# Performance work log

Measured on AMD Instinct MI355X. Metric: run time of the kernel, lower is better.

The kernel has to match this reference:

```python
import jax, jax.numpy as jnp
import numpy as np

N, MUL, NUM_ELEM = 2048, 128, 10
D_IN = 9                      # single-copy input irreps 0e+1o+2e -> 1+3+5
IN_DIMS = (1, 3, 5)           # per-irrep dims of irreps_in
OUT_DIMS = (1, 3)             # per-irrep dims of irreps_out (0e, 1o)
OUT_SLICES = ((0, 1), (1, 4)) # slices into per-mul output of width 4
# (nu, out_idx, n_basis) entries, mirroring reduced_symmetric_tensor_product_basis
ENTRIES = ((1, 0, 1), (1, 1, 1), (2, 0, 3), (2, 1, 2), (3, 0, 4), (3, 1, 2))


def setup_inputs() -> dict:
    key = jax.random.key(0)
    ks = jax.random.split(key, 2 + 2 * len(ENTRIES))
    inp = {}
    inp["node_feats"] = jax.random.normal(ks[0], (N, MUL * D_IN), dtype=jnp.float32)
    inp["species"] = jax.random.randint(ks[1], (N,), 0, NUM_ELEM)
    for i, (nu, oi, nb) in enumerate(ENTRIES):
        d = OUT_DIMS[oi]
        inp[f"basis{i}"] = jax.random.normal(ks[2 + 2 * i], (D_IN,) * nu + (nb, d), dtype=jnp.float32)
        inp[f"weight{i}"] = jax.random.normal(ks[3 + 2 * i], (NUM_ELEM, nb, MUL), dtype=jnp.float32) * (1.0 / np.sqrt(nb))
    return inp


def _to_per_mul(x):
    # (N, sum mul*dim) -> (N, mul, 9)
    pieces, off = [], 0
    for d in IN_DIMS:
        pieces.append(x[:, off:off + MUL * d].reshape(-1, MUL, d))
        off += MUL * d
    return jnp.concatenate(pieces, axis=-1)


def _from_per_mul(x):
    # (N, mul, 4) -> (N, mul*1 + mul*3)
    pieces = []
    for oi, d in enumerate(OUT_DIMS):
        lo, hi = OUT_SLICES[oi]
        pieces.append(x[:, :, lo:hi].reshape(-1, MUL * d))
    return jnp.concatenate(pieces, axis=-1)


def _forward(node_feats, bases, weights, species):
    feats = _to_per_mul(node_feats)                         # (N, mul, 9)
    out = jnp.zeros((feats.shape[0], MUL, 4), dtype=feats.dtype)
    for i, (nu, oi, nb) in enumerate(ENTRIES):
        basis = jax.lax.stop_gradient(bases[i]).astype(feats.dtype)
        tmp = jnp.einsum('a...,nma->nm...', basis, feats)   # (N, mul, 9^(nu-1), nb, d)
        for _ in range(nu - 1):
            tmp = jnp.einsum('nma...,nma->nm...', tmp, feats)
        w = weights[i][species]                             # (N, nb, mul) per-species gather
        contracted = jnp.einsum('nsm,nmsp->nmp', w, tmp)    # (N, mul, d)
        lo, hi = OUT_SLICES[oi]
        out = out.at[:, :, lo:hi].add(contracted)
    return _from_per_mul(out)


def reference(node_feats, species, basis0, weight0, basis1, weight1, basis2, weight2,
              basis3, weight3, basis4, weight4, basis5, weight5):
    bases = [basis0, basis1, basis2, basis3, basis4, basis5]
    weights = [weight0, weight1, weight2, weight3, weight4, weight5]
    return _forward(node_feats, bases, weights, species)
```

## Files before the change

### kernel.cpp

```cpp
#include <hip/hip_runtime.h>


#define N_NODES 2048
#define MUL     128
#define NROW    1152
#define NQ      45
#define NC      165
#define KSPLIT  57
#define Q4_BASE 12
#define C4_BASE 147
#define S4_TOTAL 642

__global__ void k_prep(const float* __restrict__ b0, const float* __restrict__ b1,
                       const float* __restrict__ b2, const float* __restrict__ b3,
                       const float* __restrict__ b4, const float* __restrict__ b5,
                       float4* __restrict__ S) {
    const int t = threadIdx.x;
    if (t < 9) {
        S[t] = make_float4(b0[t], b1[t * 3 + 0], b1[t * 3 + 1], b1[t * 3 + 2]);
    } else if (t < Q4_BASE) {
        S[t] = make_float4(0.f, 0.f, 0.f, 0.f);
    } else if (t < Q4_BASE + NQ) {
        const int k = t - Q4_BASE;
        int a = -1, b = -1, kk = k;
        for (int aa = 0; aa < 9 && a < 0; ++aa) {
            const int cnt = 9 - aa;
            if (kk < cnt) { a = aa; b = aa + kk; } else kk -= cnt;
        }
        const float mult = (a == b) ? 0.5f : 1.0f;
        const int i1 = a * 9 + b, i2 = b * 9 + a;
        float s2[3], s3[6];
        for (int s = 0; s < 3; ++s)
            s2[s] = (b2[i1 * 3 + s] + b2[i2 * 3 + s]) * mult;
        for (int s = 0; s < 2; ++s)
            for (int d = 0; d < 3; ++d)
                s3[s * 3 + d] = (b3[(i1 * 2 + s) * 3 + d] + b3[(i2 * 2 + s) * 3 + d]) * mult;
        S[Q4_BASE + k * 3 + 0] = make_float4(s2[0], s2[1], s2[2], 0.f);
        S[Q4_BASE + k * 3 + 1] = make_float4(s3[0], s3[1], s3[2], s3[3]);
        S[Q4_BASE + k * 3 + 2] = make_float4(s3[4], s3[5], 0.f, 0.f);
    } else if (t < Q4_BASE + NQ + NC) {
        const int k = t - Q4_BASE - NQ;
        int a = -1, b = -1, c = -1, kk = k;
        for (int aa = 0; aa < 9 && a < 0; ++aa)
            for (int bb = aa; bb < 9 && a < 0; ++bb) {
                const int cnt = 9 - bb;
                if (kk < cnt) { a = aa; b = bb; c = bb + kk; } else kk -= cnt;
            }
        const float mult = (a == b && b == c) ? (1.0f / 6.0f)
                         : ((a == b || b == c) ? 0.5f : 1.0f);
        int p[6];
        p[0] = (a * 9 + b) * 9 + c;  p[1] = (a * 9 + c) * 9 + b;
        p[2] = (b * 9 + a) * 9 + c;  p[3] = (b * 9 + c) * 9 + a;
        p[4] = (c * 9 + a) * 9 + b;  p[5] = (c * 9 + b) * 9 + a;
        float s4[4], s5[6];
        for (int s = 0; s < 4; ++s) {
            float v = 0.f;
            for (int j = 0; j < 6; ++j) v += b4[p[j] * 4 + s];
            s4[s] = v * mult;
        }
        for (int s = 0; s < 2; ++s)
            for (int d = 0; d < 3; ++d) {
                float v = 0.f;
                for (int j = 0; j < 6; ++j) v += b5[(p[j] * 2 + s) * 3 + d];
                s5[s * 3 + d] = v * mult;
            }
        S[C4_BASE + k * 3 + 0] = make_float4(s4[0], s4[1], s4[2], s4[3]);
        S[C4_BASE + k * 3 + 1] = make_float4(s5[0], s5[1], s5[2], s5[3]);
        S[C4_BASE + k * 3 + 2] = make_float4(s5[4], s5[5], 0.f, 0.f);
    }
}

typedef float fvec4 __attribute__((ext_vector_type(4)));

__global__ __launch_bounds__(256, 8) void k_eval(
        const float* __restrict__ nf, const int* __restrict__ species,
        const float* __restrict__ w0, const float* __restrict__ w1,
        const float* __restrict__ w2, const float* __restrict__ w3,
        const float* __restrict__ w4, const float* __restrict__ w5,
        const float* __restrict__ Sg, float* __restrict__ out) {
#if defined(__HIP_DEVICE_COMPILE__)
    typedef const __attribute__((address_space(4))) fvec4* S4cp;
    S4cp S = (S4cp)(unsigned long long)Sg;

    __shared__ float red[MUL * 12];

    const int tid = threadIdx.x;
    const int m = tid & 127;
    const int half = tid >> 7;
    const int n = blockIdx.x;

    const float* __restrict__ row = nf + (size_t)n * NROW;
    float f[9];
    f[0] = row[m];
#pragma unroll
    for (int j = 0; j < 3; ++j) f[1 + j] = row[128 + 3 * m + j];
#pragma unroll
    for (int j = 0; j < 5; ++j) f[4 + j] = row[512 + 5 * m + j];

    float A0 = 0.f, A1[3] = {};
    float B2[3] = {}, B3[6] = {};
    float B4[4] = {}, B5[6] = {};

    if (half == 1) {
        int kc = 0;
#pragma unroll
        for (int a = 0; a < 9; ++a) {
#pragma unroll
            for (int b = a; b < 9; ++b) {
                const float q = f[a] * f[b];
#pragma unroll
                for (int c = b; c < 9; ++c) {
                    if (kc >= KSPLIT) {
                        const fvec4 r0 = S[C4_BASE + kc * 3 + 0];
                        const fvec4 r1 = S[C4_BASE + kc * 3 + 1];
                        const fvec4 r2 = S[C4_BASE + kc * 3 + 2];
                        const float tt = q * f[c];
                        B4[0] += tt * r0.x; B4[1] += tt * r0.y;
                        B4[2] += tt * r0.z; B4[3] += tt * r0.w;
                        B5[0] += tt * r1.x; B5[1] += tt * r1.y; B5[2] += tt * r1.z;
                        B5[3] += tt * r1.w; B5[4] += tt * r2.x; B5[5] += tt * r2.y;
                    }
                    ++kc;
                }
            }
        }
        float* __restrict__ dst = &red[m * 12];
#pragma unroll
        for (int j = 0; j < 4; ++j) dst[j] = B4[j];
#pragma unroll
        for (int j = 0; j < 6; ++j) dst[4 + j] = B5[j];
    } else {
#pragma unroll
        for (int a = 0; a < 9; ++a) {
            const fvec4 L = S[a];
            A0    += L.x * f[a];
            A1[0] += L.y * f[a];
            A1[1] += L.z * f[a];
            A1[2] += L.w * f[a];
        }
        int kq = 0, kc = 0;
#pragma unroll
        for (int a = 0; a < 9; ++a) {
#pragma unroll
            for (int b = a; b < 9; ++b) {
                const float q = f[a] * f[b];
                {
                    const fvec4 r0 = S[Q4_BASE + kq * 3 + 0];
                    const fvec4 r1 = S[Q4_BASE + kq * 3 + 1];
                    const fvec4 r2 = S[Q4_BASE + kq * 3 + 2];
                    B2[0] += q * r0.x; B2[1] += q * r0.y; B2[2] += q * r0.z;
                    B3[0] += q * r1.x; B3[1] += q * r1.y; B3[2] += q * r1.z;
                    B3[3] += q * r1.w; B3[4] += q * r2.x; B3[5] += q * r2.y;
                    ++kq;
                }
#pragma unroll
                for (int c = b; c < 9; ++c) {
                    if (kc < KSPLIT) {
                        const fvec4 r0 = S[C4_BASE + kc * 3 + 0];
                        const fvec4 r1 = S[C4_BASE + kc * 3 + 1];
                        const fvec4 r2 = S[C4_BASE + kc * 3 + 2];
                        const float tt = q * f[c];
                        B4[0] += tt * r0.x; B4[1] += tt * r0.y;
                        B4[2] += tt * r0.z; B4[3] += tt * r0.w;
                        B5[0] += tt * r1.x; B5[1] += tt * r1.y; B5[2] += tt * r1.z;
                        B5[3] += tt * r1.w; B5[4] += tt * r2.x; B5[5] += tt * r2.y;
                    }
                    ++kc;
                }
            }
        }
    }

    __syncthreads();

    if (half == 0) {
        const float* __restrict__ src = &red[m * 12];
#pragma unroll
        for (int j = 0; j < 4; ++j) B4[j] += src[j];
#pragma unroll
        for (int j = 0; j < 6; ++j) B5[j] += src[4 + j];

        const int e = species[n];
        const float wv0 = w0[e * MUL + m];
        const float wv1 = w1[e * MUL + m];
        float wv2[3], wv3[2], wv4[4], wv5[2];
#pragma unroll
        for (int s = 0; s < 3; ++s) wv2[s] = w2[(e * 3 + s) * MUL + m];
#pragma unroll
        for (int s = 0; s < 2; ++s) wv3[s] = w3[(e * 2 + s) * MUL + m];
#pragma unroll
        for (int s = 0; s < 4; ++s) wv4[s] = w4[(e * 4 + s) * MUL + m];
#pragma unroll
        for (int s = 0; s < 2; ++s) wv5[s] = w5[(e * 2 + s) * MUL + m];

        float* __restrict__ orow = out + (size_t)n * 512;
        orow[m] = wv0 * A0
                + wv2[0] * B2[0] + wv2[1] * B2[1] + wv2[2] * B2[2]
                + wv4[0] * B4[0] + wv4[1] * B4[1] + wv4[2] * B4[2] + wv4[3] * B4[3];
#pragma unroll
        for (int d = 0; d < 3; ++d) {
            orow[128 + 3 * m + d] = wv1 * A1[d]
                                  + wv3[0] * B3[d] + wv3[1] * B3[3 + d]
                                  + wv5[0] * B5[d] + wv5[1] * B5[3 + d];
        }
    }
#endif
}

extern "C" void kernel_launch(void* const* d_in, const int* in_sizes, int n_in,
                              void* d_out, int out_size, void* d_ws, size_t ws_size,
                              hipStream_t stream) {
    const float* nf      = (const float*)d_in[0];
    const int*   species = (const int*)d_in[1];
    const float* b0 = (const float*)d_in[2];  const float* w0 = (const float*)d_in[3];
    const float* b1 = (const float*)d_in[4];  const float* w1 = (const float*)d_in[5];
    const float* b2 = (const float*)d_in[6];  const float* w2 = (const float*)d_in[7];
    const float* b3 = (const float*)d_in[8];  const float* w3 = (const float*)d_in[9];
    const float* b4 = (const float*)d_in[10]; const float* w4 = (const float*)d_in[11];
    const float* b5 = (const float*)d_in[12]; const float* w5 = (const float*)d_in[13];
    float* out = (float*)d_out;

    float4* S = (float4*)d_ws;

    hipLaunchKernelGGL(k_prep, dim3(1), dim3(256), 0, stream,
                       b0, b1, b2, b3, b4, b5, S);
    hipLaunchKernelGGL(k_eval, dim3(N_NODES), dim3(256), 0, stream,
                       nf, species, w0, w1, w2, w3, w4, w5,
                       (const float*)S, out);
}
```

Baseline: 108.7 us.

## Process two mul channels per thread to reuse scalar basis loads

Each thread now handles two mul channels (m and m+64) instead of one, and each block covers two nodes, so the grid is halved. Every scalar-memory basis coefficient load now feeds twice as many FMAs, which amortizes the S loads and the loop overhead. The cost is roughly double the register pressure (launch bounds lowered from 8 to 4 waves), which may reduce occupancy and latency hiding.

```diff
diff --git a/kernel.cpp b/kernel.cpp
--- a/kernel.cpp
+++ b/kernel.cpp
@@ -72,7 +72,7 @@
 
 typedef float fvec4 __attribute__((ext_vector_type(4)));
 
-__global__ __launch_bounds__(256, 8) void k_eval(
+__global__ __launch_bounds__(256, 4) void k_eval(
         const float* __restrict__ nf, const int* __restrict__ species,
         const float* __restrict__ w0, const float* __restrict__ w1,
         const float* __restrict__ w2, const float* __restrict__ w3,
@@ -82,24 +82,33 @@
     typedef const __attribute__((address_space(4))) fvec4* S4cp;
     S4cp S = (S4cp)(unsigned long long)Sg;
 
-    __shared__ float red[MUL * 12];
-
-    const int tid = threadIdx.x;
-    const int m = tid & 127;
-    const int half = tid >> 7;
-    const int n = blockIdx.x;
+    __shared__ float red[256 * 11];
+
+    const int tid  = threadIdx.x;
+    const int mp   = tid & 63;
+    const int half = (tid >> 6) & 1;
+    const int nod  = tid >> 7;
+    const int n    = (blockIdx.x << 1) | nod;
 
     const float* __restrict__ row = nf + (size_t)n * NROW;
-    float f[9];
-    f[0] = row[m];
-#pragma unroll
-    for (int j = 0; j < 3; ++j) f[1 + j] = row[128 + 3 * m + j];
-#pragma unroll
-    for (int j = 0; j < 5; ++j) f[4 + j] = row[512 + 5 * m + j];
-
-    float A0 = 0.f, A1[3] = {};
-    float B2[3] = {}, B3[6] = {};
-    float B4[4] = {}, B5[6] = {};
+    const int m0 = mp, m1 = mp + 64;
+    float f0[9], f1[9];
+    f0[0] = row[m0];
+    f1[0] = row[m1];
+#pragma unroll
+    for (int j = 0; j < 3; ++j) {
+        f0[1 + j] = row[128 + 3 * m0 + j];
+        f1[1 + j] = row[128 + 3 * m1 + j];
+    }
+#pragma unroll
+    for (int j = 0; j < 5; ++j) {
+        f0[4 + j] = row[512 + 5 * m0 + j];
+        f1[4 + j] = row[512 + 5 * m1 + j];
+    }
+
+    float A0a = 0.f, A0b = 0.f, A1a[3] = {}, A1b[3] = {};
+    float B2a[3] = {}, B2b[3] = {}, B3a[6] = {}, B3b[6] = {};
+    float B4a[4] = {}, B4b[4] = {}, B5a[6] = {}, B5b[6] = {};
 
     if (half == 1) {
         int kc = 0;
@@ -107,50 +116,69 @@
         for (int a = 0; a < 9; ++a) {
 #pragma unroll
             for (int b = a; b < 9; ++b) {
-                const float q = f[a] * f[b];
+                const float qa = f0[a] * f0[b];
+                const float qb = f1[a] * f1[b];
 #pragma unroll
                 for (int c = b; c < 9; ++c) {
                     if (kc >= KSPLIT) {
                         const fvec4 r0 = S[C4_BASE + kc * 3 + 0];
                         const fvec4 r1 = S[C4_BASE + kc * 3 + 1];
                         const fvec4 r2 = S[C4_BASE + kc * 3 + 2];
-                        const float tt = q * f[c];
-                        B4[0] += tt * r0.x; B4[1] += tt * r0.y;
-                        B4[2] += tt * r0.z; B4[3] += tt * r0.w;
-                        B5[0] += tt * r1.x; B5[1] += tt * r1.y; B5[2] += tt * r1.z;
-                        B5[3] += tt * r1.w; B5[4] += tt * r2.x; B5[5] += tt * r2.y;
+                        const float ta = qa * f0[c];
+                        const float tb = qb * f1[c];
+                        B4a[0] += ta * r0.x; B4a[1] += ta * r0.y;
+                        B4a[2] += ta * r0.z; B4a[3] += ta * r0.w;
+                        B5a[0] += ta * r1.x; B5a[1] += ta * r1.y; B5a[2] += ta * r1.z;
+                        B5a[3] += ta * r1.w; B5a[4] += ta * r2.x; B5a[5] += ta * r2.y;
+                        B4b[0] += tb * r0.x; B4b[1] += tb * r0.y;
+                        B4b[2] += tb * r0.z; B4b[3] += tb * r0.w;
+                        B5b[0] += tb * r1.x; B5b[1] += tb * r1.y; B5b[2] += tb * r1.z;
+                        B5b[3] += tb * r1.w; B5b[4] += tb * r2.x; B5b[5] += tb * r2.y;
                     }
                     ++kc;
                 }
             }
         }
-        float* __restrict__ dst = &red[m * 12];
-#pragma unroll
-        for (int j = 0; j < 4; ++j) dst[j] = B4[j];
-#pragma unroll
-        for (int j = 0; j < 6; ++j) dst[4 + j] = B5[j];
+        float* __restrict__ d0 = &red[(nod * 128 + m0) * 11];
+#pragma unroll
+        for (int j = 0; j < 4; ++j) d0[j] = B4a[j];
+#pragma unroll
+        for (int j = 0; j < 6; ++j) d0[4 + j] = B5a[j];
+        float* __restrict__ d1 = &red[(nod * 128 + m1) * 11];
+#pragma unroll
+        for (int j = 0; j < 4; ++j) d1[j] = B4b[j];
+#pragma unroll
+        for (int j = 0; j < 6; ++j) d1[4 + j] = B5b[j];
     } else {
 #pragma unroll
         for (int a = 0; a < 9; ++a) {
             const fvec4 L = S[a];
-            A0    += L.x * f[a];
-            A1[0] += L.y * f[a];
-            A1[1] += L.z * f[a];
-            A1[2] += L.w * f[a];
+            A0a    += L.x * f0[a];
+            A1a[0] += L.y * f0[a];
+            A1a[1] += L.z * f0[a];
+            A1a[2] += L.w * f0[a];
+            A0b    += L.x * f1[a];
+            A1b[0] += L.y * f1[a];
+            A1b[1] += L.z * f1[a];
+            A1b[2] += L.w * f1[a];
         }
         int kq = 0, kc = 0;
 #pragma unroll
         for (int a = 0; a < 9; ++a) {
 #pragma unroll
             for (int b = a; b < 9; ++b) {
-                const float q = f[a] * f[b];
+                const float qa = f0[a] * f0[b];
+                const float qb = f1[a] * f1[b];
                 {
                     const fvec4 r0 = S[Q4_BASE + kq * 3 + 0];
                     const fvec4 r1 = S[Q4_BASE + kq * 3 + 1];
                     const fvec4 r2 = S[Q4_BASE + kq * 3 + 2];
-                    B2[0] += q * r0.x; B2[1] += q * r0.y; B2[2] += q * r0.z;
-                    B3[0] += q * r1.x; B3[1] += q * r1.y; B3[2] += q * r1.z;
-                    B3[3] += q * r1.w; B3[4] += q * r2.x; B3[5] += q * r2.y;
+                    B2a[0] += qa * r0.x; B2a[1] += qa * r0.y; B2a[2] += qa * r0.z;
+                    B3a[0] += qa * r1.x; B3a[1] += qa * r1.y; B3a[2] += qa * r1.z;
+                    B3a[3] += qa * r1.w; B3a[4] += qa * r2.x; B3a[5] += qa * r2.y;
+                    B2b[0] += qb * r0.x; B2b[1] += qb * r0.y; B2b[2] += qb * r0.z;
+                    B3b[0] += qb * r1.x; B3b[1] += qb * r1.y; B3b[2] += qb * r1.z;
+                    B3b[3] += qb * r1.w; B3b[4] += qb * r2.x; B3b[5] += qb * r2.y;
                     ++kq;
                 }
 #pragma unroll
@@ -159,11 +187,16 @@
                         const fvec4 r0 = S[C4_BASE + kc * 3 + 0];
                         const fvec4 r1 = S[C4_BASE + kc * 3 + 1];
                         const fvec4 r2 = S[C4_BASE + kc * 3 + 2];
-                        const float tt = q * f[c];
-                        B4[0] += tt * r0.x; B4[1] += tt * r0.y;
-                        B4[2] += tt * r0.z; B4[3] += tt * r0.w;
-                        B5[0] += tt * r1.x; B5[1] += tt * r1.y; B5[2] += tt * r1.z;
-                        B5[3] += tt * r1.w; B5[4] += tt * r2.x; B5[5] += tt * r2.y;
+                        const float ta = qa * f0[c];
+                        const float tb = qb * f1[c];
+                        B4a[0] += ta * r0.x; B4a[1] += ta * r0.y;
+                        B4a[2] += ta * r0.z; B4a[3] += ta * r0.w;
+                        B5a[0] += ta * r1.x; B5a[1] += ta * r1.y; B5a[2] += ta * r1.z;
+                        B5a[3] += ta * r1.w; B5a[4] += ta * r2.x; B5a[5] += ta * r2.y;
+                        B4b[0] += tb * r0.x; B4b[1] += tb * r0.y;
+                        B4b[2] += tb * r0.z; B4b[3] += tb * r0.w;
+                        B5b[0] += tb * r1.x; B5b[1] += tb * r1.y; B5b[2] += tb * r1.z;
+                        B5b[3] += tb * r1.w; B5b[4] += tb * r2.x; B5b[5] += tb * r2.y;
                     }
                     ++kc;
                 }
@@ -174,35 +207,42 @@
     __syncthreads();
 
     if (half == 0) {
-        const float* __restrict__ src = &red[m * 12];
-#pragma unroll
-        for (int j = 0; j < 4; ++j) B4[j] += src[j];
-#pragma unroll
-        for (int j = 0; j < 6; ++j) B5[j] += src[4 + j];
-
         const int e = species[n];
-        const float wv0 = w0[e * MUL + m];
-        const float wv1 = w1[e * MUL + m];
-        float wv2[3], wv3[2], wv4[4], wv5[2];
-#pragma unroll
-        for (int s = 0; s < 3; ++s) wv2[s] = w2[(e * 3 + s) * MUL + m];
-#pragma unroll
-        for (int s = 0; s < 2; ++s) wv3[s] = w3[(e * 2 + s) * MUL + m];
-#pragma unroll
-        for (int s = 0; s < 4; ++s) wv4[s] = w4[(e * 4 + s) * MUL + m];
-#pragma unroll
-        for (int s = 0; s < 2; ++s) wv5[s] = w5[(e * 2 + s) * MUL + m];
-
         float* __restrict__ orow = out + (size_t)n * 512;
-        orow[m] = wv0 * A0
-                + wv2[0] * B2[0] + wv2[1] * B2[1] + wv2[2] * B2[2]
-                + wv4[0] * B4[0] + wv4[1] * B4[1] + wv4[2] * B4[2] + wv4[3] * B4[3];
-#pragma unroll
-        for (int d = 0; d < 3; ++d) {
-            orow[128 + 3 * m + d] = wv1 * A1[d]
-                                  + wv3[0] * B3[d] + wv3[1] * B3[3 + d]
-                                  + wv5[0] * B5[d] + wv5[1] * B5[3 + d];
-        }
+
+#define EPILOG(MM, A0v, A1v, B2v, B3v, B4v, B5v)                               \
+        do {                                                                   \
+            const float* __restrict__ src = &red[(nod * 128 + (MM)) * 11];     \
+            _Pragma("unroll")                                                  \
+            for (int j = 0; j < 4; ++j) B4v[j] += src[j];                      \
+            _Pragma("unroll")                                                  \
+            for (int j = 0; j < 6; ++j) B5v[j] += src[4 + j];                  \
+            const float wv0 = w0[e * MUL + (MM)];                              \
+            const float wv1 = w1[e * MUL + (MM)];                              \
+            float wv2[3], wv3[2], wv4[4], wv5[2];                              \
+            _Pragma("unroll")                                                  \
+            for (int s = 0; s < 3; ++s) wv2[s] = w2[(e * 3 + s) * MUL + (MM)]; \
+            _Pragma("unroll")                                                  \
+            for (int s = 0; s < 2; ++s) wv3[s] = w3[(e * 2 + s) * MUL + (MM)]; \
+            _Pragma("unroll")                                                  \
+            for (int s = 0; s < 4; ++s) wv4[s] = w4[(e * 4 + s) * MUL + (MM)]; \
+            _Pragma("unroll")                                                  \
+            for (int s = 0; s < 2; ++s) wv5[s] = w5[(e * 2 + s) * MUL + (MM)]; \
+            orow[MM] = wv0 * A0v                                               \
+                     + wv2[0] * B2v[0] + wv2[1] * B2v[1] + wv2[2] * B2v[2]     \
+                     + wv4[0] * B4v[0] + wv4[1] * B4v[1]                       \
+                     + wv4[2] * B4v[2] + wv4[3] * B4v[3];                      \
+            _Pragma("unroll")                                                  \
+            for (int d = 0; d < 3; ++d) {                                      \
+                orow[128 + 3 * (MM) + d] = wv1 * A1v[d]                        \
+                                         + wv3[0] * B3v[d] + wv3[1] * B3v[3 + d] \
+                                         + wv5[0] * B5v[d] + wv5[1] * B5v[3 + d]; \
+            }                                                                  \
+        } while (0)
+
+        EPILOG(m0, A0a, A1a, B2a, B3a, B4a, B5a);
+        EPILOG(m1, A0b, A1b, B2b, B3b, B4b, B5b);
+#undef EPILOG
     }
 #endif
 }
@@ -224,7 +264,7 @@
 
     hipLaunchKernelGGL(k_prep, dim3(1), dim3(256), 0, stream,
                        b0, b1, b2, b3, b4, b5, S);
-    hipLaunchKernelGGL(k_eval, dim3(N_NODES), dim3(256), 0, stream,
+    hipLaunchKernelGGL(k_eval, dim3(N_NODES / 2), dim3(256), 0, stream,
                        nf, species, w0, w1, w2, w3, w4, w5,
                        (const float*)S, out);
 }
```

Result: no change. 108.2 us, median of 2 (-0.5%).

## Stage symmetric basis in LDS and process two nodes per block without split

Applied to the files above, without the earlier changes.

The kernel no longer splits each node's cubic terms across two half-blocks joined by an LDS reduction. Each 128-thread half now handles a whole node, and each block covers two nodes. The precomputed basis table moves from workspace memory (read through constant-address-space scalar loads) to a device global array, which each block copies into LDS before computing. This removes the cross-half reduction and idle half, but every thread now does the full 165-term cubic loop with LDS vector loads instead of uniform scalar loads. Launch bounds drop to 4 waves-per-EU hint.

```diff
diff --git a/kernel.cpp b/kernel.cpp
--- a/kernel.cpp
+++ b/kernel.cpp
@@ -6,20 +6,20 @@
 #define NROW    1152
 #define NQ      45
 #define NC      165
-#define KSPLIT  57
 #define Q4_BASE 12
 #define C4_BASE 147
 #define S4_TOTAL 642
 
+__device__ float4 S_static[S4_TOTAL];
+
 __global__ void k_prep(const float* __restrict__ b0, const float* __restrict__ b1,
                        const float* __restrict__ b2, const float* __restrict__ b3,
-                       const float* __restrict__ b4, const float* __restrict__ b5,
-                       float4* __restrict__ S) {
+                       const float* __restrict__ b4, const float* __restrict__ b5) {
     const int t = threadIdx.x;
     if (t < 9) {
-        S[t] = make_float4(b0[t], b1[t * 3 + 0], b1[t * 3 + 1], b1[t * 3 + 2]);
+        S_static[t] = make_float4(b0[t], b1[t * 3 + 0], b1[t * 3 + 1], b1[t * 3 + 2]);
     } else if (t < Q4_BASE) {
-        S[t] = make_float4(0.f, 0.f, 0.f, 0.f);
+        S_static[t] = make_float4(0.f, 0.f, 0.f, 0.f);
     } else if (t < Q4_BASE + NQ) {
         const int k = t - Q4_BASE;
         int a = -1, b = -1, kk = k;
@@ -35,9 +35,9 @@
         for (int s = 0; s < 2; ++s)
             for (int d = 0; d < 3; ++d)
                 s3[s * 3 + d] = (b3[(i1 * 2 + s) * 3 + d] + b3[(i2 * 2 + s) * 3 + d]) * mult;
-        S[Q4_BASE + k * 3 + 0] = make_float4(s2[0], s2[1], s2[2], 0.f);
-        S[Q4_BASE + k * 3 + 1] = make_float4(s3[0], s3[1], s3[2], s3[3]);
-        S[Q4_BASE + k * 3 + 2] = make_float4(s3[4], s3[5], 0.f, 0.f);
+        S_static[Q4_BASE + k * 3 + 0] = make_float4(s2[0], s2[1], s2[2], 0.f);
+        S_static[Q4_BASE + k * 3 + 1] = make_float4(s3[0], s3[1], s3[2], s3[3]);
+        S_static[Q4_BASE + k * 3 + 2] = make_float4(s3[4], s3[5], 0.f, 0.f);
     } else if (t < Q4_BASE + NQ + NC) {
         const int k = t - Q4_BASE - NQ;
         int a = -1, b = -1, c = -1, kk = k;
@@ -64,30 +64,31 @@
                 for (int j = 0; j < 6; ++j) v += b5[(p[j] * 2 + s) * 3 + d];
                 s5[s * 3 + d] = v * mult;
             }
-        S[C4_BASE + k * 3 + 0] = make_float4(s4[0], s4[1], s4[2], s4[3]);
-        S[C4_BASE + k * 3 + 1] = make_float4(s5[0], s5[1], s5[2], s5[3]);
-        S[C4_BASE + k * 3 + 2] = make_float4(s5[4], s5[5], 0.f, 0.f);
+        S_static[C4_BASE + k * 3 + 0] = make_float4(s4[0], s4[1], s4[2], s4[3]);
+        S_static[C4_BASE + k * 3 + 1] = make_float4(s5[0], s5[1], s5[2], s5[3]);
+        S_static[C4_BASE + k * 3 + 2] = make_float4(s5[4], s5[5], 0.f, 0.f);
     }
 }
 
-typedef float fvec4 __attribute__((ext_vector_type(4)));
-
-__global__ __launch_bounds__(256, 8) void k_eval(
+__global__ __launch_bounds__(256, 4) void k_eval(
         const float* __restrict__ nf, const int* __restrict__ species,
         const float* __restrict__ w0, const float* __restrict__ w1,
         const float* __restrict__ w2, const float* __restrict__ w3,
         const float* __restrict__ w4, const float* __restrict__ w5,
-        const float* __restrict__ Sg, float* __restrict__ out) {
-#if defined(__HIP_DEVICE_COMPILE__)
-    typedef const __attribute__((address_space(4))) fvec4* S4cp;
-    S4cp S = (S4cp)(unsigned long long)Sg;
-
-    __shared__ float red[MUL * 12];
+        float* __restrict__ out) {
+    __shared__ float4 Sl[S4_TOTAL];
 
     const int tid = threadIdx.x;
-    const int m = tid & 127;
-    const int half = tid >> 7;
-    const int n = blockIdx.x;
+#pragma unroll
+    for (int i = 0; i < 3; ++i) {
+        const int idx = tid + i * 256;
+        if (idx < S4_TOTAL) Sl[idx] = S_static[idx];
+    }
+    __syncthreads();
+
+    const int m   = tid & 127;
+    const int nod = tid >> 7;
+    const int n   = (blockIdx.x << 1) | nod;
 
     const float* __restrict__ row = nf + (size_t)n * NROW;
     float f[9];
@@ -101,110 +102,68 @@
     float B2[3] = {}, B3[6] = {};
     float B4[4] = {}, B5[6] = {};
 
-    if (half == 1) {
-        int kc = 0;
 #pragma unroll
-        for (int a = 0; a < 9; ++a) {
+    for (int a = 0; a < 9; ++a) {
+        const float4 L = Sl[a];
+        A0    += L.x * f[a];
+        A1[0] += L.y * f[a];
+        A1[1] += L.z * f[a];
+        A1[2] += L.w * f[a];
+    }
+
+    int kq = 0, kc = 0;
 #pragma unroll
-            for (int b = a; b < 9; ++b) {
-                const float q = f[a] * f[b];
+    for (int a = 0; a < 9; ++a) {
 #pragma unroll
-                for (int c = b; c < 9; ++c) {
-                    if (kc >= KSPLIT) {
-                        const fvec4 r0 = S[C4_BASE + kc * 3 + 0];
-                        const fvec4 r1 = S[C4_BASE + kc * 3 + 1];
-                        const fvec4 r2 = S[C4_BASE + kc * 3 + 2];
-                        const float tt = q * f[c];
-                        B4[0] += tt * r0.x; B4[1] += tt * r0.y;
-                        B4[2] += tt * r0.z; B4[3] += tt * r0.w;
-                        B5[0] += tt * r1.x; B5[1] += tt * r1.y; B5[2] += tt * r1.z;
-                        B5[3] += tt * r1.w; B5[4] += tt * r2.x; B5[5] += tt * r2.y;
-                    }
-                    ++kc;
-                }
+        for (int b = a; b < 9; ++b) {
+            const float q = f[a] * f[b];
+            {
+                const float4 r0 = Sl[Q4_BASE + kq * 3 + 0];
+                const float4 r1 = Sl[Q4_BASE + kq * 3 + 1];
+                const float4 r2 = Sl[Q4_BASE + kq * 3 + 2];
+                B2[0] += q * r0.x; B2[1] += q * r0.y; B2[2] += q * r0.z;
+                B3[0] += q * r1.x; B3[1] += q * r1.y; B3[2] += q * r1.z;
+                B3[3] += q * r1.w; B3[4] += q * r2.x; B3[5] += q * r2.y;
+                ++kq;
             }
-        }
-        float* __restrict__ dst = &red[m * 12];
 #pragma unroll
-        for (int j = 0; j < 4; ++j) dst[j] = B4[j];
-#pragma unroll
-        for (int j = 0; j < 6; ++j) dst[4 + j] = B5[j];
-    } else {
-#pragma unroll
-        for (int a = 0; a < 9; ++a) {
-            const fvec4 L = S[a];
-            A0    += L.x * f[a];
-            A1[0] += L.y * f[a];
-            A1[1] += L.z * f[a];
-            A1[2] += L.w * f[a];
-        }
-        int kq = 0, kc = 0;
-#pragma unroll
-        for (int a = 0; a < 9; ++a) {
-#pragma unroll
-            for (int b = a; b < 9; ++b) {
-                const float q = f[a] * f[b];
-                {
-                    const fvec4 r0 = S[Q4_BASE + kq * 3 + 0];
-                    const fvec4 r1 = S[Q4_BASE + kq * 3 + 1];
-                    const fvec4 r2 = S[Q4_BASE + kq * 3 + 2];
-                    B2[0] += q * r0.x; B2[1] += q * r0.y; B2[2] += q * r0.z;
-                    B3[0] += q * r1.x; B3[1] += q * r1.y; B3[2] += q * r1.z;
-                    B3[3] += q * r1.w; B3[4] += q * r2.x; B3[5] += q * r2.y;
-                    ++kq;
-                }
-#pragma unroll
-                for (int c = b; c < 9; ++c) {
-                    if (kc < KSPLIT) {
-                        const fvec4 r0 = S[C4_BASE + kc * 3 + 0];
-                        const fvec4 r1 = S[C4_BASE + kc * 3 + 1];
-                        const fvec4 r2 = S[C4_BASE + kc * 3 + 2];
-                        const float tt = q * f[c];
-                        B4[0] += tt * r0.x; B4[1] += tt * r0.y;
-                        B4[2] += tt * r0.z; B4[3] += tt * r0.w;
-                        B5[0] += tt * r1.x; B5[1] += tt * r1.y; B5[2] += tt * r1.z;
-                        B5[3] += tt * r1.w; B5[4] += tt * r2.x; B5[5] += tt * r2.y;
-                    }
-                    ++kc;
-                }
+            for (int c = b; c < 9; ++c) {
+                const float4 r0 = Sl[C4_BASE + kc * 3 + 0];
+                const float4 r1 = Sl[C4_BASE + kc * 3 + 1];
+                const float4 r2 = Sl[C4_BASE + kc * 3 + 2];
+                const float t = q * f[c];
+                B4[0] += t * r0.x; B4[1] += t * r0.y;
+                B4[2] += t * r0.z; B4[3] += t * r0.w;
+                B5[0] += t * r1.x; B5[1] += t * r1.y; B5[2] += t * r1.z;
+                B5[3] += t * r1.w; B5[4] += t * r2.x; B5[5] += t * r2.y;
+                ++kc;
             }
         }
     }
 
-    __syncthreads();
+    const int e = species[n];
+    const float wv0 = w0[e * MUL + m];
+    const float wv1 = w1[e * MUL + m];
+    float wv2[3], wv3[2], wv4[4], wv5[2];
+#pragma unroll
+    for (int s = 0; s < 3; ++s) wv2[s] = w2[(e * 3 + s) * MUL + m];
+#pragma unroll
+    for (int s = 0; s < 2; ++s) wv3[s] = w3[(e * 2 + s) * MUL + m];
+#pragma unroll
+    for (int s = 0; s < 4; ++s) wv4[s] = w4[(e * 4 + s) * MUL + m];
+#pragma unroll
+    for (int s = 0; s < 2; ++s) wv5[s] = w5[(e * 2 + s) * MUL + m];
 
-    if (half == 0) {
-        const float* __restrict__ src = &red[m * 12];
+    float* __restrict__ orow = out + (size_t)n * 512;
+    orow[m] = wv0 * A0
+            + wv2[0] * B2[0] + wv2[1] * B2[1] + wv2[2] * B2[2]
+            + wv4[0] * B4[0] + wv4[1] * B4[1] + wv4[2] * B4[2] + wv4[3] * B4[3];
 #pragma unroll
-        for (int j = 0; j < 4; ++j) B4[j] += src[j];
-#pragma unroll
-        for (int j = 0; j < 6; ++j) B5[j] += src[4 + j];
-
-        const int e = species[n];
-        const float wv0 = w0[e * MUL + m];
-        const float wv1 = w1[e * MUL + m];
-        float wv2[3], wv3[2], wv4[4], wv5[2];
-#pragma unroll
-        for (int s = 0; s < 3; ++s) wv2[s] = w2[(e * 3 + s) * MUL + m];
-#pragma unroll
-        for (int s = 0; s < 2; ++s) wv3[s] = w3[(e * 2 + s) * MUL + m];
-#pragma unroll
-        for (int s = 0; s < 4; ++s) wv4[s] = w4[(e * 4 + s) * MUL + m];
-#pragma unroll
-        for (int s = 0; s < 2; ++s) wv5[s] = w5[(e * 2 + s) * MUL + m];
-
-        float* __restrict__ orow = out + (size_t)n * 512;
-        orow[m] = wv0 * A0
-                + wv2[0] * B2[0] + wv2[1] * B2[1] + wv2[2] * B2[2]
-                + wv4[0] * B4[0] + wv4[1] * B4[1] + wv4[2] * B4[2] + wv4[3] * B4[3];
-#pragma unroll
-        for (int d = 0; d < 3; ++d) {
-            orow[128 + 3 * m + d] = wv1 * A1[d]
-                                  + wv3[0] * B3[d] + wv3[1] * B3[3 + d]
-                                  + wv5[0] * B5[d] + wv5[1] * B5[3 + d];
-        }
+    for (int d = 0; d < 3; ++d) {
+        orow[128 + 3 * m + d] = wv1 * A1[d]
+                              + wv3[0] * B3[d] + wv3[1] * B3[3 + d]
+                              + wv5[0] * B5[d] + wv5[1] * B5[3 + d];
     }
-#endif
 }
 
 extern "C" void kernel_launch(void* const* d_in, const int* in_sizes, int n_in,
@@ -220,11 +179,10 @@
     const float* b5 = (const float*)d_in[12]; const float* w5 = (const float*)d_in[13];
     float* out = (float*)d_out;
 
-    float4* S = (float4*)d_ws;
+    (void)d_ws; (void)ws_size;
 
     hipLaunchKernelGGL(k_prep, dim3(1), dim3(256), 0, stream,
-                       b0, b1, b2, b3, b4, b5, S);
-    hipLaunchKernelGGL(k_eval, dim3(N_NODES), dim3(256), 0, stream,
-                       nf, species, w0, w1, w2, w3, w4, w5,
-                       (const float*)S, out);
+                       b0, b1, b2, b3, b4, b5);
+    hipLaunchKernelGGL(k_eval, dim3(N_NODES / 2), dim3(256), 0, stream,
+                       nf, species, w0, w1, w2, w3, w4, w5, out);
 }
```

New measurement: 120.6 us. 10.9% more time.
